# Kernel tuning notes

Measured on AMD Instinct MI355X. Metric: run time of the kernel, lower is better.

The kernel has to match this reference:

```python
import jax, jax.numpy as jnp
import numpy as np

NUM_HEADS = 16
ROPE_BASE = 10000.0


def _rope_cos_sin(seq_len, head_dim, dtype):
    inv_freq = 1.0 / (ROPE_BASE ** (jnp.arange(0, head_dim, 2, dtype=jnp.float32) / head_dim))
    freqs = jnp.arange(seq_len, dtype=jnp.float32)[:, None] * inv_freq[None, :]  # [L, hd/2]
    return jnp.cos(freqs).astype(dtype), jnp.sin(freqs).astype(dtype)


def _apply_rope(t, cos, sin):
    # t: [B, H, L, hd]; cos/sin: [L, hd/2] broadcast over B,H
    x1 = t[..., ::2]
    x2 = t[..., 1::2]
    r1 = x1 * cos - x2 * sin
    r2 = x1 * sin + x2 * cos
    return jnp.stack([r1, r2], axis=-1).reshape(t.shape)


def setup_inputs() -> dict:
    key = jax.random.key(0)
    k1, k2, k3 = jax.random.split(key, 3)
    B, L, D = 2, 2048, 1024
    x = jax.random.normal(k1, (B, L, D), dtype=jnp.float32)
    W_qkv = jax.random.normal(k2, (3 * D, D), dtype=jnp.float32) * (D ** -0.5)
    W_out = jax.random.normal(k3, (D, D), dtype=jnp.float32) * (D ** -0.5)
    return {"x": x, "W_qkv": W_qkv, "W_out": W_out}


def reference(x, W_qkv, W_out):
    B, L, D = x.shape
    H = NUM_HEADS
    hd = D // H
    scale = hd ** -0.5

    qkv = x @ W_qkv.T                              # [B, L, 3D]
    qkv = qkv.reshape(B, L, 3, H, hd)
    qkv = jnp.transpose(qkv, (2, 0, 3, 1, 4))      # [3, B, H, L, hd]
    q, k, v = qkv[0], qkv[1], qkv[2]

    cos, sin = _rope_cos_sin(L, hd, x.dtype)
    q = _apply_rope(q, cos, sin)
    k = _apply_rope(k, cos, sin)

    logits = jnp.einsum("bhqd,bhkd->bhqk", q, k) * scale
    attn = jax.nn.softmax(logits, axis=-1)         # dropout p=0.0 -> identity
    out = jnp.einsum("bhqk,bhkd->bhqd", attn, v)   # [B, H, L, hd]
    out = jnp.transpose(out, (0, 2, 1, 3)).reshape(B, L, D)
    return out @ W_out.T
```

## Files before the change

kernel.cpp:

```cpp
#include <hip/hip_runtime.h>
#include <hip/hip_bf16.h>
#include <stdint.h>


typedef __bf16 bf16x8 __attribute__((ext_vector_type(8)));
typedef float f32x4 __attribute__((ext_vector_type(4)));

__device__ __forceinline__ unsigned short f2bf(float f) {
  union { float f; unsigned int u; } v; v.f = f;
  unsigned int r = v.u + 0x7FFFu + ((v.u >> 16) & 1u);
  return (unsigned short)(r >> 16);
}
__device__ __forceinline__ float b2f(unsigned short u) {
  union { unsigned int u; float f; } v; v.u = ((unsigned int)u) << 16;
  return v.f;
}

__device__ __forceinline__ void gl2lds16(const void* gptr, void* lptr) {
  __builtin_amdgcn_global_load_lds(
      (const __attribute__((address_space(1))) unsigned int*)gptr,
      (__attribute__((address_space(3))) unsigned int*)lptr, 16, 0, 0);
}

__global__ void cvt_all(const float4* __restrict__ x,
                        const float4* __restrict__ wq,
                        const float4* __restrict__ wo,
                        ushort4* __restrict__ xb,
                        ushort4* __restrict__ wqb,
                        ushort4* __restrict__ wob) {
  int i = blockIdx.x * 256 + threadIdx.x;
  float4 v; ushort4* dst; int j;
  if (i < 1048576)      { v = x[i];            dst = xb;  j = i; }
  else if (i < 1835008) { v = wq[i - 1048576]; dst = wqb; j = i - 1048576; }
  else                  { v = wo[i - 1835008]; dst = wob; j = i - 1835008; }
  ushort4 o;
  o.x = f2bf(v.x); o.y = f2bf(v.y); o.z = f2bf(v.z); o.w = f2bf(v.w);
  dst[j] = o;
}

template<int OUT_MODE>
__global__ __launch_bounds__(256) void gemm_bt(
    const __hip_bfloat16* __restrict__ A,
    const __hip_bfloat16* __restrict__ B,
    void* __restrict__ C, int M, int N, int K, int Ksplit) {
  __shared__ __align__(16) __hip_bfloat16 As[128 * 32];
  __shared__ __align__(16) __hip_bfloat16 Bs[128 * 32];
  const int tid = threadIdx.x;
  const int lane = tid & 63;
  const int wave = tid >> 6;
  const int wm = (wave >> 1) * 64, wn = (wave & 1) * 64;
  const int g = lane >> 4, lr = lane & 15;
  const int m0 = blockIdx.y * 128, n0 = blockIdx.x * 128;
  const int kbeg = blockIdx.z * Ksplit;
  f32x4 acc[4][4] = {};

  const char* Ag = (const char*)(A + (size_t)m0 * K);
  const char* Bg = (const char*)(B + (size_t)n0 * K);
  const size_t ldb = (size_t)K * 2;

  for (int kt = kbeg; kt < kbeg + Ksplit; kt += 32) {
    const char* Ak = Ag + (size_t)kt * 2;
    const char* Bk = Bg + (size_t)kt * 2;
#pragma unroll
    for (int j = 0; j < 2; ++j) {
      int c = tid + j * 256;
      int row = c >> 2;
      int colb = (c & 3) * 16;
      gl2lds16(Ak + (size_t)row * ldb + colb, (char*)As + c * 16);
      gl2lds16(Bk + (size_t)row * ldb + colb, (char*)Bs + c * 16);
    }
    asm volatile("s_waitcnt vmcnt(0)" ::: "memory");
    __syncthreads();
    bf16x8 af[4], bfr[4];
#pragma unroll
    for (int i = 0; i < 4; ++i)
      af[i] = *(const bf16x8*)((const char*)As + (size_t)(wm + i * 16 + lr) * 64 + g * 16);
#pragma unroll
    for (int i = 0; i < 4; ++i)
      bfr[i] = *(const bf16x8*)((const char*)Bs + (size_t)(wn + i * 16 + lr) * 64 + g * 16);
#pragma unroll
    for (int i = 0; i < 4; ++i)
#pragma unroll
      for (int j = 0; j < 4; ++j)
        acc[i][j] = __builtin_amdgcn_mfma_f32_16x16x32_bf16(af[i], bfr[j], acc[i][j], 0, 0, 0);
    __syncthreads();
  }

#pragma unroll
  for (int i = 0; i < 4; ++i) {
#pragma unroll
    for (int j = 0; j < 4; ++j) {
      int n = n0 + wn + j * 16 + lr;
#pragma unroll
      for (int r = 0; r < 4; ++r) {
        int m = m0 + wm + i * 16 + g * 4 + r;
        float v = acc[i][j][r];
        if (OUT_MODE == 1) {
          ((unsigned short*)C)[(size_t)m * N + n] = f2bf(v);
        } else if (OUT_MODE == 2) {
          unsafeAtomicAdd(&((float*)C)[(size_t)m * N + n], v);
        } else {
          ((float*)C)[(size_t)m * N + n] = v;
        }
      }
    }
  }
}

__global__ void rope_scatter(const __hip_bfloat16* __restrict__ qkv,
                             __hip_bfloat16* __restrict__ Qs,
                             __hip_bfloat16* __restrict__ Ks,
                             __hip_bfloat16* __restrict__ Vt) {
  const int t = blockIdx.x * 256 + threadIdx.x;
  const int i = t & 31;
  const int lc = (t >> 5) & 255;
  const int h = (t >> 13) & 15;
  const int b = t >> 17;
  const float inv_freq = powf(10000.0f, -(float)i * (1.0f / 32.0f));
  const float QSCALE = 0.125f * 1.44269504088896f;
  const unsigned short* qk = (const unsigned short*)qkv;
  unsigned short v0[8], v1[8];
#pragma unroll
  for (int j = 0; j < 8; ++j) {
    const int l = lc * 8 + j;
    const size_t row = ((size_t)(b * 2048 + l)) * 3072;
    float s, c;
    sincosf((float)l * inv_freq, &s, &c);
    ushort2 qp = *(const ushort2*)(qk + row + h * 64 + 2 * i);
    ushort2 kp = *(const ushort2*)(qk + row + 1024 + h * 64 + 2 * i);
    ushort2 vp = *(const ushort2*)(qk + row + 2048 + h * 64 + 2 * i);
    float x1 = b2f(qp.x), x2 = b2f(qp.y);
    float y1 = b2f(kp.x), y2 = b2f(kp.y);
    size_t oidx = (((size_t)(b * 16 + h)) * 2048 + l) * 64 + 2 * i;
    ushort2 qo, ko;
    qo.x = f2bf((x1 * c - x2 * s) * QSCALE);
    qo.y = f2bf((x1 * s + x2 * c) * QSCALE);
    ko.x = f2bf(y1 * c - y2 * s);
    ko.y = f2bf(y1 * s + y2 * c);
    *(ushort2*)((unsigned short*)Qs + oidx) = qo;
    *(ushort2*)((unsigned short*)Ks + oidx) = ko;
    v0[j] = vp.x; v1[j] = vp.y;
  }
  const int m = lc & 3;
  const int colA = ((m & 1) << 4) + ((m >> 1) << 2);
  unsigned short* Vtu = (unsigned short*)Vt;
  const size_t vrow0 = (((size_t)(b * 16 + h)) * 64 + 2 * i) * 2048 + (lc >> 2) * 32;
  const size_t vrow1 = vrow0 + 2048;
  *(ushort4*)(Vtu + vrow0 + colA)     = make_ushort4(v0[0], v0[1], v0[2], v0[3]);
  *(ushort4*)(Vtu + vrow0 + colA + 8) = make_ushort4(v0[4], v0[5], v0[6], v0[7]);
  *(ushort4*)(Vtu + vrow1 + colA)     = make_ushort4(v1[0], v1[1], v1[2], v1[3]);
  *(ushort4*)(Vtu + vrow1 + colA + 8) = make_ushort4(v1[4], v1[5], v1[6], v1[7]);
}

__global__ __launch_bounds__(256, 4) void attn_fwd(
    const __hip_bfloat16* __restrict__ Qs,
    const __hip_bfloat16* __restrict__ Ks,
    const __hip_bfloat16* __restrict__ Vt,
    float* __restrict__ Opart,
    float2* __restrict__ Ml) {
  constexpr int L = 2048;
  __shared__ __align__(16) char lds[32768];
  const int tid = threadIdx.x, lane = tid & 63, w = tid >> 6;
  const int g = lane >> 4, lr = lane & 15;
  const int blk = blockIdx.x;
  const int xcd = blk & 7, slot = blk >> 3;
  const int bh = xcd * 4 + (slot >> 5);
  const int rem = slot & 31;
  const int qt = rem >> 1, half = rem & 1;
  const int q0 = qt * 128 + w * 32 + lr;
  const int kt0 = half * 16;

  const __hip_bfloat16* Qr = Qs + ((size_t)bh * L + q0) * 64;
  bf16x8 qf[2][2];
  qf[0][0] = *(const bf16x8*)(Qr + g * 8);
  qf[0][1] = *(const bf16x8*)(Qr + 32 + g * 8);
  qf[1][0] = *(const bf16x8*)(Qr + 16 * 64 + g * 8);
  qf[1][1] = *(const bf16x8*)(Qr + 16 * 64 + 32 + g * 8);

  bf16x8 onesf;
#pragma unroll
  for (int j = 0; j < 8; ++j) onesf[j] = (__bf16)1.0f;

  const int xmask = (lr & 7) << 4;
  const int loff0 = ((g * 16) ^ (xmask & 0x30)) + (xmask & 0x40);
  const int kb0 = lr * 128 + loff0;
  const int kb1 = kb0 ^ 64;

  const int c0 = tid * 16, c1 = c0 + 4096;
  const int os0 = c0 ^ (((c0 >> 7) & 7) << 4);
  const int os1 = c1 ^ (((c1 >> 7) & 7) << 4);
  const char* Kb = (const char*)(Ks + (size_t)bh * L * 64) + (size_t)kt0 * 8192;
  const char* Vb = (const char*)(Vt + (size_t)bh * 64 * L) + kt0 * 128;
  const char* KsrcA = Kb + os0;
  const char* KsrcB = Kb + os1;
  const char* VsrcA = Vb + (size_t)(os0 >> 7) * (L * 2) + (os0 & 127);
  const char* VsrcB = Vb + (size_t)(os1 >> 7) * (L * 2) + (os1 & 127);

  auto stage = [&](int bo) {
    gl2lds16(KsrcA, lds + bo + c0);
    gl2lds16(KsrcB, lds + bo + c1);
    gl2lds16(VsrcA, lds + 16384 + bo + c0);
    gl2lds16(VsrcB, lds + 16384 + bo + c1);
    KsrcA += 8192; KsrcB += 8192; VsrcA += 128; VsrcB += 128;
  };

  f32x4 oacc[2][4] = {};
  f32x4 lacc[2] = {};
  float mrun[2] = {-1e30f, -1e30f};

  stage(0);

  for (int kt = 0; kt < 16; ++kt) {
    const int bo = (kt & 1) * 8192;
    if (kt + 1 < 16) {
      stage(bo ^ 8192);
      asm volatile("s_waitcnt vmcnt(4)" ::: "memory");
    } else {
      asm volatile("s_waitcnt vmcnt(0)" ::: "memory");
    }
    __builtin_amdgcn_s_barrier();

    const char* Kc = lds + bo;
    const char* Vc = lds + 16384 + bo;

    f32x4 sacc[2][4] = {};
    __builtin_amdgcn_s_setprio(1);
#pragma unroll
    for (int mf = 0; mf < 4; ++mf) {
      bf16x8 a0 = *(const bf16x8*)(Kc + kb0 + mf * 2048);
      bf16x8 a1 = *(const bf16x8*)(Kc + kb1 + mf * 2048);
      sacc[0][mf] = __builtin_amdgcn_mfma_f32_16x16x32_bf16(a0, qf[0][0], sacc[0][mf], 0, 0, 0);
      sacc[0][mf] = __builtin_amdgcn_mfma_f32_16x16x32_bf16(a1, qf[0][1], sacc[0][mf], 0, 0, 0);
      sacc[1][mf] = __builtin_amdgcn_mfma_f32_16x16x32_bf16(a0, qf[1][0], sacc[1][mf], 0, 0, 0);
      sacc[1][mf] = __builtin_amdgcn_mfma_f32_16x16x32_bf16(a1, qf[1][1], sacc[1][mf], 0, 0, 0);
    }
    __builtin_amdgcn_s_setprio(0);

#pragma unroll
    for (int qg = 0; qg < 2; ++qg) {
      float a0 = fmaxf(fmaxf(sacc[qg][0][0], sacc[qg][0][1]), sacc[qg][0][2]);
      float a1 = fmaxf(fmaxf(sacc[qg][0][3], sacc[qg][1][0]), sacc[qg][1][1]);
      float a2 = fmaxf(fmaxf(sacc[qg][1][2], sacc[qg][1][3]), sacc[qg][2][0]);
      float a3 = fmaxf(fmaxf(sacc[qg][2][1], sacc[qg][2][2]), sacc[qg][2][3]);
      float a4 = fmaxf(fmaxf(sacc[qg][3][0], sacc[qg][3][1]), sacc[qg][3][2]);
      float b0 = fmaxf(fmaxf(a0, a1), a2);
      float b1 = fmaxf(fmaxf(a3, a4), sacc[qg][3][3]);
      float lmax = fmaxf(b0, b1);
      if (__any(lmax > mrun[qg] + 8.0f)) {
        float tmax = fmaxf(lmax, __shfl_xor(lmax, 16));
        tmax = fmaxf(tmax, __shfl_xor(tmax, 32));
        float mnew = fmaxf(mrun[qg], tmax);
        float al = __builtin_amdgcn_exp2f(mrun[qg] - mnew);
        mrun[qg] = mnew;
        lacc[qg] *= al;
#pragma unroll
        for (int d = 0; d < 4; ++d) oacc[qg][d] = oacc[qg][d] * al;
      }
#pragma unroll
      for (int mf = 0; mf < 4; ++mf) {
        sacc[qg][mf][0] = __builtin_amdgcn_exp2f(sacc[qg][mf][0] - mrun[qg]);
        sacc[qg][mf][1] = __builtin_amdgcn_exp2f(sacc[qg][mf][1] - mrun[qg]);
        sacc[qg][mf][2] = __builtin_amdgcn_exp2f(sacc[qg][mf][2] - mrun[qg]);
        sacc[qg][mf][3] = __builtin_amdgcn_exp2f(sacc[qg][mf][3] - mrun[qg]);
      }
    }

#pragma unroll
    for (int ks = 0; ks < 2; ++ks) {
      bf16x8 pf[2];
#pragma unroll
      for (int qg = 0; qg < 2; ++qg) {
#pragma unroll
        for (int j = 0; j < 4; ++j) {
          pf[qg][j]     = (__bf16)sacc[qg][2 * ks][j];
          pf[qg][4 + j] = (__bf16)sacc[qg][2 * ks + 1][j];
        }
      }
      const int kb = ks ? kb1 : kb0;
      __builtin_amdgcn_s_setprio(1);
      lacc[0] = __builtin_amdgcn_mfma_f32_16x16x32_bf16(onesf, pf[0], lacc[0], 0, 0, 0);
      lacc[1] = __builtin_amdgcn_mfma_f32_16x16x32_bf16(onesf, pf[1], lacc[1], 0, 0, 0);
#pragma unroll
      for (int df = 0; df < 4; ++df) {
        bf16x8 a = *(const bf16x8*)(Vc + kb + df * 2048);
        oacc[0][df] = __builtin_amdgcn_mfma_f32_16x16x32_bf16(a, pf[0], oacc[0][df], 0, 0, 0);
        oacc[1][df] = __builtin_amdgcn_mfma_f32_16x16x32_bf16(a, pf[1], oacc[1][df], 0, 0, 0);
      }
      __builtin_amdgcn_s_setprio(0);
    }
    asm volatile("s_waitcnt lgkmcnt(0)" ::: "memory");
    __builtin_amdgcn_s_barrier();
  }

#pragma unroll
  for (int qg = 0; qg < 2; ++qg) {
    const size_t rowi = ((size_t)bh * L + q0 + qg * 16) * 2 + half;
    float* Od = Opart + rowi * 64;
#pragma unroll
    for (int df = 0; df < 4; ++df)
      *(f32x4*)(Od + df * 16 + g * 4) = oacc[qg][df];
    if (g == 0) {
      float2 ml; ml.x = mrun[qg]; ml.y = lacc[qg][0];
      Ml[rowi] = ml;
    }
  }
}

__global__ __launch_bounds__(256) void attn_reduce(
    const float* __restrict__ Opart, const float2* __restrict__ Ml,
    unsigned short* __restrict__ Ob) {
  int t = blockIdx.x * 256 + threadIdx.x;
  int d = t & 63;
  int r = t >> 6;
  float2 a = Ml[2 * r], b = Ml[2 * r + 1];
  float m = fmaxf(a.x, b.x);
  float w0 = __builtin_amdgcn_exp2f(a.x - m);
  float w1 = __builtin_amdgcn_exp2f(b.x - m);
  float l = a.y * w0 + b.y * w1;
  float o = Opart[(size_t)(2 * r) * 64 + d] * w0 + Opart[(size_t)(2 * r + 1) * 64 + d] * w1;
  float out = o / l;
  int bh = r >> 11, qq = r & 2047;
  Ob[(((size_t)(bh >> 4) * 2048 + qq)) * 1024 + (bh & 15) * 64 + d] = f2bf(out);
}

extern "C" void kernel_launch(void* const* d_in, const int* in_sizes, int n_in,
                              void* d_out, int out_size, void* d_ws, size_t ws_size,
                              hipStream_t stream) {
  (void)in_sizes; (void)n_in; (void)ws_size;
  const float* x    = (const float*)d_in[0];
  const float* wqkv = (const float*)d_in[1];
  const float* wout = (const float*)d_in[2];

  char* ws = (char*)d_ws;
  auto* wob   = (__hip_bfloat16*)(ws + ((size_t)0u  << 20));
  auto* Qsb   = (__hip_bfloat16*)(ws + ((size_t)2u  << 20));
  auto* Ob    = (__hip_bfloat16*)(ws + ((size_t)2u  << 20));
  auto* Ksb   = (__hip_bfloat16*)(ws + ((size_t)10u << 20));
  auto* Vtb   = (__hip_bfloat16*)(ws + ((size_t)18u << 20));
  auto* qkvb  = (__hip_bfloat16*)(ws + ((size_t)26u << 20));
  auto* Opart = (float*)         (ws + ((size_t)26u << 20));
  auto* xb    = (__hip_bfloat16*)(ws + ((size_t)50u << 20));
  auto* wqb   = (__hip_bfloat16*)(ws + ((size_t)58u << 20));
  auto* Mlp   = (float2*)        (ws + ((size_t)58u << 20));

  cvt_all<<<8192, 256, 0, stream>>>((const float4*)x, (const float4*)wqkv,
                                    (const float4*)wout,
                                    (ushort4*)xb, (ushort4*)wqb, (ushort4*)wob);
  gemm_bt<1><<<dim3(24, 32, 1), 256, 0, stream>>>(xb, wqb, (void*)qkvb,
                                                  4096, 3072, 1024, 1024);
  rope_scatter<<<1024, 256, 0, stream>>>(qkvb, Qsb, Ksb, Vtb);
  attn_fwd<<<1024, 256, 0, stream>>>(Qsb, Ksb, Vtb, Opart, Mlp);
  attn_reduce<<<16384, 256, 0, stream>>>(Opart, Mlp, (unsigned short*)Ob);
  hipMemsetAsync(d_out, 0, (size_t)out_size * sizeof(float), stream);
  gemm_bt<2><<<dim3(8, 32, 2), 256, 0, stream>>>(Ob, wob, d_out,
                                                 4096, 1024, 1024, 512);
}
```

Baseline: 160.1 us.

## Replace split-K atomic output GEMM with double-buffered 64x64 tile kernel

The output projection no longer uses a split-K GEMM that needs a memset plus atomic float adds. A new 64x64-tile kernel launches 1024 blocks and stores fp32 directly. It double-buffers LDS loads via global_load_lds, swizzles LDS addresses to avoid bank conflicts, and raises wave priority around the MFMAs. This removes the memset launch and atomic traffic, but each wave computes a smaller tile, so operands get less reuse.

Measured after the change: 137.3 us. 1.17x faster.

```diff
diff --git a/kernel.cpp b/kernel.cpp
--- a/kernel.cpp
+++ b/kernel.cpp
@@ -38,11 +38,10 @@
   dst[j] = o;
 }
 
-template<int OUT_MODE>
 __global__ __launch_bounds__(256) void gemm_bt(
     const __hip_bfloat16* __restrict__ A,
     const __hip_bfloat16* __restrict__ B,
-    void* __restrict__ C, int M, int N, int K, int Ksplit) {
+    unsigned short* __restrict__ C, int M, int N, int K) {
   __shared__ __align__(16) __hip_bfloat16 As[128 * 32];
   __shared__ __align__(16) __hip_bfloat16 Bs[128 * 32];
   const int tid = threadIdx.x;
@@ -51,14 +50,13 @@
   const int wm = (wave >> 1) * 64, wn = (wave & 1) * 64;
   const int g = lane >> 4, lr = lane & 15;
   const int m0 = blockIdx.y * 128, n0 = blockIdx.x * 128;
-  const int kbeg = blockIdx.z * Ksplit;
   f32x4 acc[4][4] = {};
 
   const char* Ag = (const char*)(A + (size_t)m0 * K);
   const char* Bg = (const char*)(B + (size_t)n0 * K);
   const size_t ldb = (size_t)K * 2;
 
-  for (int kt = kbeg; kt < kbeg + Ksplit; kt += 32) {
+  for (int kt = 0; kt < K; kt += 32) {
     const char* Ak = Ag + (size_t)kt * 2;
     const char* Bk = Bg + (size_t)kt * 2;
 #pragma unroll
@@ -94,15 +92,68 @@
 #pragma unroll
       for (int r = 0; r < 4; ++r) {
         int m = m0 + wm + i * 16 + g * 4 + r;
-        float v = acc[i][j][r];
-        if (OUT_MODE == 1) {
-          ((unsigned short*)C)[(size_t)m * N + n] = f2bf(v);
-        } else if (OUT_MODE == 2) {
-          unsafeAtomicAdd(&((float*)C)[(size_t)m * N + n], v);
-        } else {
-          ((float*)C)[(size_t)m * N + n] = v;
-        }
+        C[(size_t)m * N + n] = f2bf(acc[i][j][r]);
       }
+    }
+  }
+}
+
+__global__ __launch_bounds__(256) void gemm2_64(
+    const __hip_bfloat16* __restrict__ A,
+    const __hip_bfloat16* __restrict__ B,
+    float* __restrict__ C, int M, int N, int K) {
+  __shared__ __align__(16) char lds[16384];
+  const int tid = threadIdx.x, lane = tid & 63, w = tid >> 6;
+  const int g = lane >> 4, lr = lane & 15;
+  const int n0 = blockIdx.x * 64, m0 = blockIdx.y * 64;
+  f32x4 acc[4] = {};
+
+  const size_t ld = (size_t)K * 2;
+  const int o16 = tid * 16;
+  const int s = o16 ^ (((o16 >> 6) & 3) << 4);
+  const int srow = s >> 6, scolb = s & 63;
+  const char* Asrc = (const char*)(A + (size_t)m0 * K) + (size_t)srow * ld + scolb;
+  const char* Bsrc = (const char*)(B + (size_t)n0 * K) + (size_t)srow * ld + scolb;
+
+  auto stage = [&](int bo) {
+    gl2lds16(Asrc, lds + bo + o16);
+    gl2lds16(Bsrc, lds + 8192 + bo + o16);
+    Asrc += 64; Bsrc += 64;
+  };
+
+  stage(0);
+
+  const int swz = (lr & 3) << 4;
+  const int NSTEP = K / 32;
+  for (int kt = 0; kt < NSTEP; ++kt) {
+    const int bo = (kt & 1) * 4096;
+    if (kt + 1 < NSTEP) {
+      stage(bo ^ 4096);
+      asm volatile("s_waitcnt vmcnt(2)" ::: "memory");
+    } else {
+      asm volatile("s_waitcnt vmcnt(0)" ::: "memory");
+    }
+    __builtin_amdgcn_s_barrier();
+
+    bf16x8 af = *(const bf16x8*)(lds + bo + (((w * 16 + lr) * 64 + g * 16) ^ swz));
+    __builtin_amdgcn_s_setprio(1);
+#pragma unroll
+    for (int j = 0; j < 4; ++j) {
+      bf16x8 bf = *(const bf16x8*)(lds + 8192 + bo + (((j * 16 + lr) * 64 + g * 16) ^ swz));
+      acc[j] = __builtin_amdgcn_mfma_f32_16x16x32_bf16(af, bf, acc[j], 0, 0, 0);
+    }
+    __builtin_amdgcn_s_setprio(0);
+    asm volatile("s_waitcnt lgkmcnt(0)" ::: "memory");
+    __builtin_amdgcn_s_barrier();
+  }
+
+#pragma unroll
+  for (int j = 0; j < 4; ++j) {
+    int n = n0 + j * 16 + lr;
+#pragma unroll
+    for (int r = 0; r < 4; ++r) {
+      int m = m0 + w * 16 + g * 4 + r;
+      C[(size_t)m * N + n] = acc[j][r];
     }
   }
 }
@@ -326,7 +377,7 @@
 extern "C" void kernel_launch(void* const* d_in, const int* in_sizes, int n_in,
                               void* d_out, int out_size, void* d_ws, size_t ws_size,
                               hipStream_t stream) {
-  (void)in_sizes; (void)n_in; (void)ws_size;
+  (void)in_sizes; (void)n_in; (void)out_size; (void)ws_size;
   const float* x    = (const float*)d_in[0];
   const float* wqkv = (const float*)d_in[1];
   const float* wout = (const float*)d_in[2];
@@ -346,12 +397,11 @@
   cvt_all<<<8192, 256, 0, stream>>>((const float4*)x, (const float4*)wqkv,
                                     (const float4*)wout,
                                     (ushort4*)xb, (ushort4*)wqb, (ushort4*)wob);
-  gemm_bt<1><<<dim3(24, 32, 1), 256, 0, stream>>>(xb, wqb, (void*)qkvb,
-                                                  4096, 3072, 1024, 1024);
+  gemm_bt<<<dim3(24, 32), 256, 0, stream>>>(xb, wqb, (unsigned short*)qkvb,
+                                            4096, 3072, 1024);
   rope_scatter<<<1024, 256, 0, stream>>>(qkvb, Qsb, Ksb, Vtb);
   attn_fwd<<<1024, 256, 0, stream>>>(Qsb, Ksb, Vtb, Opart, Mlp);
   attn_reduce<<<16384, 256, 0, stream>>>(Opart, Mlp, (unsigned short*)Ob);
-  hipMemsetAsync(d_out, 0, (size_t)out_size * sizeof(float), stream);
-  gemm_bt<2><<<dim3(8, 32, 2), 256, 0, stream>>>(Ob, wob, d_out,
-                                                 4096, 1024, 1024, 512);
-}
+  gemm2_64<<<dim3(16, 64), 256, 0, stream>>>(Ob, wob, (float*)d_out,
+                                             4096, 1024, 1024);
+}
```
